# Kernel optimization log

Hardware: AMD Instinct MI355X
Metric: run time of the kernel (lower is better)

## Reference

```python
import jax, jax.numpy as jnp
import numpy as np
import math

B, S, D, H = 1, 2048, 4096, 32
HD = D // H
FF = 11008
EPS = 1e-5
THETA = 10000.0


def rms_norm(x, w, eps=EPS):
    # use_mean=False, elementwise_scale=True, high-precision pow -> RMSNorm in fp32
    xf = x.astype(jnp.float32)
    inv = jax.lax.rsqrt(jnp.mean(xf * xf, axis=-1, keepdims=True) + eps)
    return ((xf * inv).astype(x.dtype)) * w


def rope(x, theta=THETA):
    # x: [b, s, h, hd]; interleaved (adjacent-pair) rotary as in LLaMA/FMS
    s, hd = x.shape[1], x.shape[-1]
    inv_freq = 1.0 / (theta ** (jnp.arange(0, hd, 2, dtype=jnp.float32) / hd))
    ang = jnp.arange(s, dtype=jnp.float32)[:, None] * inv_freq[None, :]  # [s, hd/2]
    cos = jnp.cos(ang)[None, :, None, :].astype(x.dtype)
    sin = jnp.sin(ang)[None, :, None, :].astype(x.dtype)
    x1 = x[..., 0::2]
    x2 = x[..., 1::2]
    r1 = x1 * cos - x2 * sin
    r2 = x1 * sin + x2 * cos
    return jnp.stack([r1, r2], axis=-1).reshape(x.shape)


def block_forward(x, ln_w, ff_ln_w, wq, wk, wv, wo, wg, w1, w2):
    residual = x
    xn = rms_norm(x, ln_w)
    b, s, d = xn.shape
    q = rope((xn @ wq).reshape(b, s, H, HD))
    k = rope((xn @ wk).reshape(b, s, H, HD))
    v = (xn @ wv).reshape(b, s, H, HD)
    scores = jnp.einsum('bqhd,bkhd->bhqk', q, k) / math.sqrt(HD)
    causal = jnp.tril(jnp.ones((s, s), dtype=bool))
    scores = jnp.where(causal[None, None], scores, jnp.finfo(scores.dtype).min)
    probs = jax.nn.softmax(scores, axis=-1)
    attn = jnp.einsum('bhqk,bkhd->bqhd', probs, v).reshape(b, s, d)
    x = attn @ wo + residual

    residual = x
    xn = rms_norm(x, ff_ln_w)
    h = jax.nn.silu(xn @ wg) * (xn @ w1)  # swish-gated GLU
    x = h @ w2 + residual
    return x


def setup_inputs() -> dict:
    key = jax.random.key(0)
    ks = jax.random.split(key, 8)
    sc = lambda fan_in: 1.0 / math.sqrt(fan_in)
    return {
        'x': jax.random.normal(ks[0], (B, S, D), jnp.float32),
        'ln_w': jnp.ones((D,), jnp.float32),
        'ff_ln_w': jnp.ones((D,), jnp.float32),
        'wq': jax.random.normal(ks[1], (D, D), jnp.float32) * sc(D),
        'wk': jax.random.normal(ks[2], (D, D), jnp.float32) * sc(D),
        'wv': jax.random.normal(ks[3], (D, D), jnp.float32) * sc(D),
        'wo': jax.random.normal(ks[4], (D, D), jnp.float32) * sc(D),
        'wg': jax.random.normal(ks[5], (D, FF), jnp.float32) * sc(D),
        'w1': jax.random.normal(ks[6], (D, FF), jnp.float32) * sc(D),
        'w2': jax.random.normal(ks[7], (FF, D), jnp.float32) * sc(FF),
    }


def reference(x, ln_w, ff_ln_w, wq, wk, wv, wo, wg, w1, w2):
    return block_forward(x, ln_w, ff_ln_w, wq, wk, wv, wo, wg, w1, w2)
```

## Files before the change

kernel.cpp:

```cpp
#include <hip/hip_runtime.h>
#include <cstdint>
#include <cmath>


typedef unsigned short u16;
typedef unsigned int u32;
typedef __bf16 bf16x8 __attribute__((ext_vector_type(8)));
typedef float f32x4 __attribute__((ext_vector_type(4)));

__device__ __forceinline__ float bf2f(u16 u) {
    u32 x = ((u32)u) << 16; float f; __builtin_memcpy(&f, &x, 4); return f;
}
__device__ __forceinline__ u16 f2bf(float f) {
    u32 x; __builtin_memcpy(&x, &f, 4);
    u32 r = x + 0x7fff + ((x >> 16) & 1);
    return (u16)(r >> 16);
}

__device__ __forceinline__ void g2l16(const void* g, void* l) {
    auto* gp = reinterpret_cast<const u32*>(reinterpret_cast<uintptr_t>(g));
    auto* lp = reinterpret_cast<__attribute__((address_space(3))) u32*>(
        reinterpret_cast<uintptr_t>(l));
    __builtin_amdgcn_global_load_lds(gp, lp, 16, 0, 0);
}

__global__ __launch_bounds__(256) void transpose_f32_bf16(
    const float* __restrict__ in, u16* __restrict__ out, int K, int N) {
    __shared__ float tile[64][33];
    const int k0 = blockIdx.y * 64, n0 = blockIdx.x * 32;
    const int x = threadIdx.x, y = threadIdx.y;
#pragma unroll
    for (int i = 0; i < 8; i++) {
        int kr = y + i * 8;
        tile[kr][x] = in[(size_t)(k0 + kr) * N + n0 + x];
    }
    __syncthreads();
#pragma unroll
    for (int i = 0; i < 4; i++) {
        int nr = y + i * 8;
        u32 pk = (u32)f2bf(tile[2 * x][nr]) | ((u32)f2bf(tile[2 * x + 1][nr]) << 16);
        ((u32*)(out + (size_t)(n0 + nr) * K + k0))[x] = pk;
    }
}

__global__ __launch_bounds__(256) void rmsnorm_kernel(
    const float* __restrict__ x, const float* __restrict__ w, u16* __restrict__ o) {
    const int row = blockIdx.x;
    const float4* xr = (const float4*)(x + (size_t)row * 4096);
    float4 v[4];
    float ss = 0.f;
#pragma unroll
    for (int i = 0; i < 4; i++) {
        v[i] = xr[threadIdx.x + 256 * i];
        ss += v[i].x * v[i].x + v[i].y * v[i].y + v[i].z * v[i].z + v[i].w * v[i].w;
    }
#pragma unroll
    for (int off = 32; off > 0; off >>= 1) ss += __shfl_down(ss, off, 64);
    __shared__ float ws4[4];
    if ((threadIdx.x & 63) == 0) ws4[threadIdx.x >> 6] = ss;
    __syncthreads();
    float inv = rsqrtf((ws4[0] + ws4[1] + ws4[2] + ws4[3]) * (1.f / 4096.f) + 1e-5f);
    const float4* wr = (const float4*)w;
    u32* orow = (u32*)(o + (size_t)row * 4096);
#pragma unroll
    for (int i = 0; i < 4; i++) {
        float4 wv = wr[threadIdx.x + 256 * i];
        u32 lo = (u32)f2bf(v[i].x * inv * wv.x) | ((u32)f2bf(v[i].y * inv * wv.y) << 16);
        u32 hi = (u32)f2bf(v[i].z * inv * wv.z) | ((u32)f2bf(v[i].w * inv * wv.w) << 16);
        int idx = (threadIdx.x + 256 * i) * 2;
        orow[idx] = lo; orow[idx + 1] = hi;
    }
}

__global__ __launch_bounds__(256) void rope_kernel(u16* __restrict__ q, u16* __restrict__ k) {
    const int s = blockIdx.x;
    u32* pr = (u32*)((blockIdx.y ? k : q) + (size_t)s * 4096);
#pragma unroll
    for (int it = 0; it < 8; it++) {
        int pidx = threadIdx.x + it * 256;
        int i = pidx & 63;
        float ang = (float)s * expf(-(float)i * 0.14391156832817f);
        float sn, cs; sincosf(ang, &sn, &cs);
        u32 u = pr[pidx];
        float x1 = bf2f((u16)u), x2 = bf2f((u16)(u >> 16));
        pr[pidx] = (u32)f2bf(x1 * cs - x2 * sn) | ((u32)f2bf(x1 * sn + x2 * cs) << 16);
    }
}

__global__ __launch_bounds__(256) void silu_mul_kernel(
    const u16* __restrict__ g, const u16* __restrict__ u, u16* __restrict__ o) {
    size_t i = (size_t)blockIdx.x * 256 + threadIdx.x;
    uint4 gv = ((const uint4*)g)[i];
    uint4 uv = ((const uint4*)u)[i];
    const u32* gp = (const u32*)&gv;
    const u32* up = (const u32*)&uv;
    u32 rr[4];
#pragma unroll
    for (int j = 0; j < 4; j++) {
        float g0 = bf2f((u16)gp[j]), g1 = bf2f((u16)(gp[j] >> 16));
        float u0 = bf2f((u16)up[j]), u1 = bf2f((u16)(up[j] >> 16));
        float s0 = g0 / (1.f + __expf(-g0)) * u0;
        float s1 = g1 / (1.f + __expf(-g1)) * u1;
        rr[j] = (u32)f2bf(s0) | ((u32)f2bf(s1) << 16);
    }
    ((uint4*)o)[i] = *(const uint4*)rr;
}

template <int EPI>
__global__ __launch_bounds__(256) void gemm_bt(
    const u16* __restrict__ A, const u16* __restrict__ BT, void* __restrict__ Cout,
    const float* __restrict__ res, int M, int N, int K, int lda, int ldb, int ldc) {
    (void)M; (void)N;
    __shared__ u16 As[128 * 32];
    __shared__ u16 Bs[128 * 32];
    const int tid = threadIdx.x;
    const int lane = tid & 63, wave = tid >> 6;
    const int m0 = blockIdx.y * 128, n0 = blockIdx.x * 128;
    const int wm = (wave >> 1) * 64, wn = (wave & 1) * 64;
    const int gc = lane & 15, grp = lane >> 4;

    const u16* ga0 = A + (size_t)(m0 + (tid >> 2)) * lda + (tid & 3) * 8;
    const u16* ga1 = ga0 + (size_t)64 * lda;
    const u16* gb0 = BT + (size_t)(n0 + (tid >> 2)) * ldb + (tid & 3) * 8;
    const u16* gb1 = gb0 + (size_t)64 * ldb;
    u16* la0 = As + tid * 8;
    u16* la1 = As + tid * 8 + 2048;
    u16* lb0 = Bs + tid * 8;
    u16* lb1 = Bs + tid * 8 + 2048;

    f32x4 acc[4][4] = {};

    for (int k0 = 0; k0 < K; k0 += 32) {
        g2l16(ga0, la0); g2l16(ga1, la1);
        g2l16(gb0, lb0); g2l16(gb1, lb1);
        ga0 += 32; ga1 += 32; gb0 += 32; gb1 += 32;
        __syncthreads();
        bf16x8 af[4], bfr[4];
#pragma unroll
        for (int t = 0; t < 4; t++) {
            af[t]  = *(const bf16x8*)(As + (wm + t * 16 + gc) * 32 + grp * 8);
            bfr[t] = *(const bf16x8*)(Bs + (wn + t * 16 + gc) * 32 + grp * 8);
        }
#pragma unroll
        for (int mt = 0; mt < 4; mt++)
#pragma unroll
            for (int nt = 0; nt < 4; nt++)
                acc[mt][nt] = __builtin_amdgcn_mfma_f32_16x16x32_bf16(
                    af[mt], bfr[nt], acc[mt][nt], 0, 0, 0);
        __syncthreads();
    }

#pragma unroll
    for (int mt = 0; mt < 4; mt++) {
#pragma unroll
        for (int nt = 0; nt < 4; nt++) {
            int row0 = m0 + wm + mt * 16 + grp * 4;
            int col = n0 + wn + nt * 16 + gc;
            if (EPI == 0) {
                u16* C = (u16*)Cout;
#pragma unroll
                for (int r = 0; r < 4; r++)
                    C[(size_t)(row0 + r) * ldc + col] = f2bf(acc[mt][nt][r]);
            } else if (EPI == 1) {
                u16* C = (u16*)Cout;
                u32 p0 = (u32)f2bf(acc[mt][nt][0]) | ((u32)f2bf(acc[mt][nt][1]) << 16);
                u32 p1 = (u32)f2bf(acc[mt][nt][2]) | ((u32)f2bf(acc[mt][nt][3]) << 16);
                u32* dst = (u32*)(C + (size_t)col * ldc + row0);
                dst[0] = p0; dst[1] = p1;
            } else {
                float* C = (float*)Cout;
#pragma unroll
                for (int r = 0; r < 4; r++) {
                    size_t idx = (size_t)(row0 + r) * ldc + col;
                    C[idx] = acc[mt][nt][r] + res[idx];
                }
            }
        }
    }
}

__global__ __launch_bounds__(256) void attn_kernel(
    const u16* __restrict__ q, const u16* __restrict__ k,
    const u16* __restrict__ vt, u16* __restrict__ o) {
    __shared__ u16 Ks[64][136];
    __shared__ u16 Vs[128][72];
    __shared__ u16 Ps[128][72];
    const int h = blockIdx.y;
    const int m0 = blockIdx.x * 128;
    const int tid = threadIdx.x, lane = tid & 63, wave = tid >> 6;
    const int mw = m0 + wave * 32;
    const int gc = lane & 15, grp = lane >> 4;
    const float scale = 0.08838834764831843f;

    bf16x8 qf[2][4];
#pragma unroll
    for (int mt = 0; mt < 2; mt++)
#pragma unroll
        for (int ks = 0; ks < 4; ks++)
            qf[mt][ks] = *(const bf16x8*)(q + (size_t)(mw + mt * 16 + gc) * 4096 +
                                          h * 128 + ks * 32 + grp * 8);

    f32x4 oacc[2][8] = {};
    float mrun[2][4], lrun[2][4];
#pragma unroll
    for (int mt = 0; mt < 2; mt++)
#pragma unroll
        for (int r = 0; r < 4; r++) { mrun[mt][r] = -1e30f; lrun[mt][r] = 0.f; }

    const int jend = m0 + 128;
    for (int j0 = 0; j0 < jend; j0 += 64) {
#pragma unroll
        for (int i = 0; i < 4; i++) {
            int c = tid + i * 256;
            int kr = c >> 4, dc = (c & 15) * 8;
            *(uint4*)(&Ks[kr][dc]) =
                *(const uint4*)(k + (size_t)(j0 + kr) * 4096 + h * 128 + dc);
            int vr = c >> 3, vc = (c & 7) * 8;
            *(uint4*)(&Vs[vr][vc]) =
                *(const uint4*)(vt + (size_t)(h * 128 + vr) * 2048 + j0 + vc);
        }
        __syncthreads();

        f32x4 sfr[2][4] = {};
#pragma unroll
        for (int ks = 0; ks < 4; ks++) {
            bf16x8 kf[4];
#pragma unroll
            for (int nt = 0; nt < 4; nt++)
                kf[nt] = *(const bf16x8*)(&Ks[nt * 16 + gc][ks * 32 + grp * 8]);
#pragma unroll
            for (int mt = 0; mt < 2; mt++)
#pragma unroll
                for (int nt = 0; nt < 4; nt++)
                    sfr[mt][nt] = __builtin_amdgcn_mfma_f32_16x16x32_bf16(
                        qf[mt][ks], kf[nt], sfr[mt][nt], 0, 0, 0);
        }

        if (j0 + 63 > mw) {
#pragma unroll
            for (int mt = 0; mt < 2; mt++)
#pragma unroll
                for (int nt = 0; nt < 4; nt++)
#pragma unroll
                    for (int r = 0; r < 4; r++) {
                        int rowg = mw + mt * 16 + grp * 4 + r;
                        int colg = j0 + nt * 16 + gc;
                        if (colg > rowg) sfr[mt][nt][r] = -3.0e38f;
                    }
        }

#pragma unroll
        for (int mt = 0; mt < 2; mt++) {
#pragma unroll
            for (int r = 0; r < 4; r++) {
                float rm = fmaxf(fmaxf(sfr[mt][0][r], sfr[mt][1][r]),
                                 fmaxf(sfr[mt][2][r], sfr[mt][3][r])) * scale;
#pragma unroll
                for (int msk = 1; msk < 16; msk <<= 1)
                    rm = fmaxf(rm, __shfl_xor(rm, msk, 64));
                float mnew = fmaxf(mrun[mt][r], rm);
                float alpha = __expf(mrun[mt][r] - mnew);
                mrun[mt][r] = mnew;
                float rs = 0.f;
#pragma unroll
                for (int nt = 0; nt < 4; nt++) {
                    float pv = __expf(sfr[mt][nt][r] * scale - mnew);
                    sfr[mt][nt][r] = pv;
                    rs += pv;
                }
#pragma unroll
                for (int msk = 1; msk < 16; msk <<= 1) rs += __shfl_xor(rs, msk, 64);
                lrun[mt][r] = lrun[mt][r] * alpha + rs;
#pragma unroll
                for (int nd = 0; nd < 8; nd++) oacc[mt][nd][r] *= alpha;
            }
        }

#pragma unroll
        for (int mt = 0; mt < 2; mt++)
#pragma unroll
            for (int nt = 0; nt < 4; nt++)
#pragma unroll
                for (int r = 0; r < 4; r++)
                    Ps[wave * 32 + mt * 16 + grp * 4 + r][nt * 16 + gc] =
                        f2bf(sfr[mt][nt][r]);
        __syncthreads();

#pragma unroll
        for (int ks2 = 0; ks2 < 2; ks2++) {
            bf16x8 pf[2];
#pragma unroll
            for (int mt = 0; mt < 2; mt++)
                pf[mt] = *(const bf16x8*)(&Ps[wave * 32 + mt * 16 + gc][ks2 * 32 + grp * 8]);
#pragma unroll
            for (int nd = 0; nd < 8; nd++) {
                bf16x8 vf = *(const bf16x8*)(&Vs[nd * 16 + gc][ks2 * 32 + grp * 8]);
#pragma unroll
                for (int mt = 0; mt < 2; mt++)
                    oacc[mt][nd] = __builtin_amdgcn_mfma_f32_16x16x32_bf16(
                        pf[mt], vf, oacc[mt][nd], 0, 0, 0);
            }
        }
        __syncthreads();
    }

#pragma unroll
    for (int mt = 0; mt < 2; mt++)
#pragma unroll
        for (int r = 0; r < 4; r++) {
            float invl = 1.f / lrun[mt][r];
            int rowg = mw + mt * 16 + grp * 4 + r;
#pragma unroll
            for (int nd = 0; nd < 8; nd++)
                o[(size_t)rowg * 4096 + h * 128 + nd * 16 + gc] =
                    f2bf(oacc[mt][nd][r] * invl);
        }
}

extern "C" void kernel_launch(void* const* d_in, const int* in_sizes, int n_in,
                              void* d_out, int out_size, void* d_ws, size_t ws_size,
                              hipStream_t stream) {
    (void)in_sizes; (void)n_in; (void)out_size; (void)ws_size;
    const float* x    = (const float*)d_in[0];
    const float* ln_w = (const float*)d_in[1];
    const float* ffw  = (const float*)d_in[2];
    const float* wq   = (const float*)d_in[3];
    const float* wk   = (const float*)d_in[4];
    const float* wv   = (const float*)d_in[5];
    const float* wo   = (const float*)d_in[6];
    const float* wg   = (const float*)d_in[7];
    const float* w1   = (const float*)d_in[8];
    const float* w2   = (const float*)d_in[9];
    float* out = (float*)d_out;

    char* p = (char*)d_ws;
    auto alloc = [&](size_t n) { char* r = p; p += (n + 255) & ~(size_t)255; return r; };
    u16* wqT = (u16*)alloc((size_t)4096 * 4096 * 2);
    u16* wkT = (u16*)alloc((size_t)4096 * 4096 * 2);
    u16* wvT = (u16*)alloc((size_t)4096 * 4096 * 2);
    u16* woT = (u16*)alloc((size_t)4096 * 4096 * 2);
    u16* wgT = (u16*)alloc((size_t)11008 * 4096 * 2);
    u16* w1T = (u16*)alloc((size_t)11008 * 4096 * 2);
    u16* w2T = (u16*)alloc((size_t)4096 * 11008 * 2);
    u16* xn  = (u16*)alloc((size_t)2048 * 4096 * 2);
    u16* qb  = (u16*)alloc((size_t)2048 * 4096 * 2);
    u16* kb  = (u16*)alloc((size_t)2048 * 4096 * 2);
    u16* vtb = (u16*)alloc((size_t)4096 * 2048 * 2);
    u16* ab  = (u16*)alloc((size_t)2048 * 4096 * 2);
    float* x2 = (float*)alloc((size_t)2048 * 4096 * 4);
    u16* xn2 = (u16*)alloc((size_t)2048 * 4096 * 2);
    u16* gb  = (u16*)alloc((size_t)2048 * 11008 * 2);
    u16* ub  = (u16*)alloc((size_t)2048 * 11008 * 2);

    dim3 tb(32, 8);
    transpose_f32_bf16<<<dim3(128, 64), tb, 0, stream>>>(wq, wqT, 4096, 4096);
    transpose_f32_bf16<<<dim3(128, 64), tb, 0, stream>>>(wk, wkT, 4096, 4096);
    transpose_f32_bf16<<<dim3(128, 64), tb, 0, stream>>>(wv, wvT, 4096, 4096);
    transpose_f32_bf16<<<dim3(128, 64), tb, 0, stream>>>(wo, woT, 4096, 4096);
    transpose_f32_bf16<<<dim3(344, 64), tb, 0, stream>>>(wg, wgT, 4096, 11008);
    transpose_f32_bf16<<<dim3(344, 64), tb, 0, stream>>>(w1, w1T, 4096, 11008);
    transpose_f32_bf16<<<dim3(128, 172), tb, 0, stream>>>(w2, w2T, 11008, 4096);

    rmsnorm_kernel<<<2048, 256, 0, stream>>>(x, ln_w, xn);

    gemm_bt<0><<<dim3(32, 16), 256, 0, stream>>>(xn, wqT, qb, nullptr,
                                                 2048, 4096, 4096, 4096, 4096, 4096);
    gemm_bt<0><<<dim3(32, 16), 256, 0, stream>>>(xn, wkT, kb, nullptr,
                                                 2048, 4096, 4096, 4096, 4096, 4096);
    gemm_bt<1><<<dim3(32, 16), 256, 0, stream>>>(xn, wvT, vtb, nullptr,
                                                 2048, 4096, 4096, 4096, 4096, 2048);

    rope_kernel<<<dim3(2048, 2), 256, 0, stream>>>(qb, kb);

    attn_kernel<<<dim3(16, 32), 256, 0, stream>>>(qb, kb, vtb, ab);

    gemm_bt<2><<<dim3(32, 16), 256, 0, stream>>>(ab, woT, x2, x,
                                                 2048, 4096, 4096, 4096, 4096, 4096);

    rmsnorm_kernel<<<2048, 256, 0, stream>>>(x2, ffw, xn2);

    gemm_bt<0><<<dim3(86, 16), 256, 0, stream>>>(xn2, wgT, gb, nullptr,
                                                 2048, 11008, 4096, 4096, 4096, 11008);
    gemm_bt<0><<<dim3(86, 16), 256, 0, stream>>>(xn2, w1T, ub, nullptr,
                                                 2048, 11008, 4096, 4096, 4096, 11008);

    silu_mul_kernel<<<11008, 256, 0, stream>>>(gb, ub, gb);

    gemm_bt<2><<<dim3(32, 16), 256, 0, stream>>>(gb, w2T, out, x2,
                                                 2048, 4096, 11008, 11008, 11008, 4096);
}
```

Before: 2.421 ms.

## Pair causal attention tiles per block with double-buffered K/V and 8 waves

The attention kernel now gives each block two query tiles (ti and 15-ti), so every block does a roughly equal amount of causal work. It uses 512 threads with 16 rows per wave and double-buffers K/V in shared memory, loading the next tile into registers while the current one is computed. This also drops one barrier per iteration. The aim is to remove load imbalance from the causal mask and hide global load latency, at the cost of more shared memory and half as many blocks (256) on the device.

```diff
diff --git a/kernel.cpp b/kernel.cpp
--- a/kernel.cpp
+++ b/kernel.cpp
@@ -179,142 +179,166 @@
     }
 }
 
-__global__ __launch_bounds__(256) void attn_kernel(
+__global__ __launch_bounds__(512) void attn_kernel(
     const u16* __restrict__ q, const u16* __restrict__ k,
     const u16* __restrict__ vt, u16* __restrict__ o) {
-    __shared__ u16 Ks[64][136];
-    __shared__ u16 Vs[128][72];
+    __shared__ u16 Ks[2][64][136];
+    __shared__ u16 Vs[2][128][72];
     __shared__ u16 Ps[128][72];
     const int h = blockIdx.y;
-    const int m0 = blockIdx.x * 128;
     const int tid = threadIdx.x, lane = tid & 63, wave = tid >> 6;
-    const int mw = m0 + wave * 32;
     const int gc = lane & 15, grp = lane >> 4;
     const float scale = 0.08838834764831843f;
 
-    bf16x8 qf[2][4];
-#pragma unroll
-    for (int mt = 0; mt < 2; mt++)
-#pragma unroll
-        for (int ks = 0; ks < 4; ks++)
-            qf[mt][ks] = *(const bf16x8*)(q + (size_t)(mw + mt * 16 + gc) * 4096 +
-                                          h * 128 + ks * 32 + grp * 8);
-
-    f32x4 oacc[2][8] = {};
-    float mrun[2][4], lrun[2][4];
-#pragma unroll
-    for (int mt = 0; mt < 2; mt++)
-#pragma unroll
-        for (int r = 0; r < 4; r++) { mrun[mt][r] = -1e30f; lrun[mt][r] = 0.f; }
-
-    const int jend = m0 + 128;
-    for (int j0 = 0; j0 < jend; j0 += 64) {
-#pragma unroll
-        for (int i = 0; i < 4; i++) {
-            int c = tid + i * 256;
-            int kr = c >> 4, dc = (c & 15) * 8;
-            *(uint4*)(&Ks[kr][dc]) =
-                *(const uint4*)(k + (size_t)(j0 + kr) * 4096 + h * 128 + dc);
-            int vr = c >> 3, vc = (c & 7) * 8;
-            *(uint4*)(&Vs[vr][vc]) =
-                *(const uint4*)(vt + (size_t)(h * 128 + vr) * 2048 + j0 + vc);
-        }
-        __syncthreads();
-
-        f32x4 sfr[2][4] = {};
+    const int ti0 = blockIdx.x;
+    const int ti1 = 15 - (int)blockIdx.x;
+    const int n0 = 2 * ti0 + 2;
+    const int total = n0 + 2 * ti1 + 2;
+
+    {
+        uint4 kr0[2], vr0[2];
+#pragma unroll
+        for (int i = 0; i < 2; i++) {
+            int c = tid + i * 512;
+            kr0[i] = *(const uint4*)(k + (size_t)(c >> 4) * 4096 + h * 128 + (c & 15) * 8);
+            vr0[i] = *(const uint4*)(vt + (size_t)(h * 128 + (c >> 3)) * 2048 + (c & 7) * 8);
+        }
+#pragma unroll
+        for (int i = 0; i < 2; i++) {
+            int c = tid + i * 512;
+            *(uint4*)(&Ks[0][c >> 4][(c & 15) * 8]) = kr0[i];
+            *(uint4*)(&Vs[0][c >> 3][(c & 7) * 8]) = vr0[i];
+        }
+    }
+    __syncthreads();
+
+    bf16x8 qf[4];
+    f32x4 oacc[8];
+    float mrun[4], lrun[4];
+    const f32x4 fzero = {};
+    int cur = 0;
+
+    for (int it = 0; it < total; ++it) {
+        const int t = (it >= n0) ? 1 : 0;
+        const int local = t ? it - n0 : it;
+        const int ti = t ? ti1 : ti0;
+        const int j0 = local * 64;
+        const int mw = ti * 128 + wave * 16;
+
+        if (local == 0) {
+#pragma unroll
+            for (int ks = 0; ks < 4; ks++)
+                qf[ks] = *(const bf16x8*)(q + (size_t)(mw + gc) * 4096 + h * 128 +
+                                          ks * 32 + grp * 8);
+#pragma unroll
+            for (int nd = 0; nd < 8; nd++) oacc[nd] = fzero;
+#pragma unroll
+            for (int r = 0; r < 4; r++) { mrun[r] = -1e30f; lrun[r] = 0.f; }
+        }
+
+        const int itn = it + 1;
+        const bool havenext = itn < total;
+        const int jn = (itn >= n0 ? itn - n0 : itn) * 64;
+        uint4 kreg[2], vreg[2];
+        if (havenext) {
+#pragma unroll
+            for (int i = 0; i < 2; i++) {
+                int c = tid + i * 512;
+                kreg[i] = *(const uint4*)(k + (size_t)(jn + (c >> 4)) * 4096 +
+                                          h * 128 + (c & 15) * 8);
+                vreg[i] = *(const uint4*)(vt + (size_t)(h * 128 + (c >> 3)) * 2048 +
+                                          jn + (c & 7) * 8);
+            }
+        }
+
+        f32x4 sfr[4] = {};
 #pragma unroll
         for (int ks = 0; ks < 4; ks++) {
             bf16x8 kf[4];
 #pragma unroll
             for (int nt = 0; nt < 4; nt++)
-                kf[nt] = *(const bf16x8*)(&Ks[nt * 16 + gc][ks * 32 + grp * 8]);
-#pragma unroll
-            for (int mt = 0; mt < 2; mt++)
-#pragma unroll
-                for (int nt = 0; nt < 4; nt++)
-                    sfr[mt][nt] = __builtin_amdgcn_mfma_f32_16x16x32_bf16(
-                        qf[mt][ks], kf[nt], sfr[mt][nt], 0, 0, 0);
+                kf[nt] = *(const bf16x8*)(&Ks[cur][nt * 16 + gc][ks * 32 + grp * 8]);
+#pragma unroll
+            for (int nt = 0; nt < 4; nt++)
+                sfr[nt] = __builtin_amdgcn_mfma_f32_16x16x32_bf16(
+                    qf[ks], kf[nt], sfr[nt], 0, 0, 0);
         }
 
         if (j0 + 63 > mw) {
 #pragma unroll
-            for (int mt = 0; mt < 2; mt++)
-#pragma unroll
-                for (int nt = 0; nt < 4; nt++)
-#pragma unroll
-                    for (int r = 0; r < 4; r++) {
-                        int rowg = mw + mt * 16 + grp * 4 + r;
-                        int colg = j0 + nt * 16 + gc;
-                        if (colg > rowg) sfr[mt][nt][r] = -3.0e38f;
-                    }
-        }
-
-#pragma unroll
-        for (int mt = 0; mt < 2; mt++) {
+            for (int nt = 0; nt < 4; nt++)
+#pragma unroll
+                for (int r = 0; r < 4; r++) {
+                    int rowg = mw + grp * 4 + r;
+                    int colg = j0 + nt * 16 + gc;
+                    if (colg > rowg) sfr[nt][r] = -3.0e38f;
+                }
+        }
+
+#pragma unroll
+        for (int r = 0; r < 4; r++) {
+            float rm = fmaxf(fmaxf(sfr[0][r], sfr[1][r]),
+                             fmaxf(sfr[2][r], sfr[3][r])) * scale;
+#pragma unroll
+            for (int msk = 1; msk < 16; msk <<= 1)
+                rm = fmaxf(rm, __shfl_xor(rm, msk, 64));
+            float mnew = fmaxf(mrun[r], rm);
+            float alpha = __expf(mrun[r] - mnew);
+            mrun[r] = mnew;
+            float rs = 0.f;
+#pragma unroll
+            for (int nt = 0; nt < 4; nt++) {
+                float pv = __expf(sfr[nt][r] * scale - mnew);
+                sfr[nt][r] = pv;
+                rs += pv;
+            }
+#pragma unroll
+            for (int msk = 1; msk < 16; msk <<= 1) rs += __shfl_xor(rs, msk, 64);
+            lrun[r] = lrun[r] * alpha + rs;
+#pragma unroll
+            for (int nd = 0; nd < 8; nd++) oacc[nd][r] *= alpha;
+        }
+
+#pragma unroll
+        for (int nt = 0; nt < 4; nt++)
+#pragma unroll
+            for (int r = 0; r < 4; r++)
+                Ps[wave * 16 + grp * 4 + r][nt * 16 + gc] = f2bf(sfr[nt][r]);
+
+#pragma unroll
+        for (int ks2 = 0; ks2 < 2; ks2++) {
+            bf16x8 pf = *(const bf16x8*)(&Ps[wave * 16 + gc][ks2 * 32 + grp * 8]);
+#pragma unroll
+            for (int nd = 0; nd < 8; nd++) {
+                bf16x8 vf = *(const bf16x8*)(&Vs[cur][nd * 16 + gc][ks2 * 32 + grp * 8]);
+                oacc[nd] = __builtin_amdgcn_mfma_f32_16x16x32_bf16(
+                    pf, vf, oacc[nd], 0, 0, 0);
+            }
+        }
+
+        if (havenext) {
+#pragma unroll
+            for (int i = 0; i < 2; i++) {
+                int c = tid + i * 512;
+                *(uint4*)(&Ks[cur ^ 1][c >> 4][(c & 15) * 8]) = kreg[i];
+                *(uint4*)(&Vs[cur ^ 1][c >> 3][(c & 7) * 8]) = vreg[i];
+            }
+        }
+        __syncthreads();
+        cur ^= 1;
+
+        if (local == 2 * ti + 1) {
 #pragma unroll
             for (int r = 0; r < 4; r++) {
-                float rm = fmaxf(fmaxf(sfr[mt][0][r], sfr[mt][1][r]),
-                                 fmaxf(sfr[mt][2][r], sfr[mt][3][r])) * scale;
-#pragma unroll
-                for (int msk = 1; msk < 16; msk <<= 1)
-                    rm = fmaxf(rm, __shfl_xor(rm, msk, 64));
-                float mnew = fmaxf(mrun[mt][r], rm);
-                float alpha = __expf(mrun[mt][r] - mnew);
-                mrun[mt][r] = mnew;
-                float rs = 0.f;
-#pragma unroll
-                for (int nt = 0; nt < 4; nt++) {
-                    float pv = __expf(sfr[mt][nt][r] * scale - mnew);
-                    sfr[mt][nt][r] = pv;
-                    rs += pv;
-                }
-#pragma unroll
-                for (int msk = 1; msk < 16; msk <<= 1) rs += __shfl_xor(rs, msk, 64);
-                lrun[mt][r] = lrun[mt][r] * alpha + rs;
-#pragma unroll
-                for (int nd = 0; nd < 8; nd++) oacc[mt][nd][r] *= alpha;
-            }
-        }
-
-#pragma unroll
-        for (int mt = 0; mt < 2; mt++)
-#pragma unroll
-            for (int nt = 0; nt < 4; nt++)
-#pragma unroll
-                for (int r = 0; r < 4; r++)
-                    Ps[wave * 32 + mt * 16 + grp * 4 + r][nt * 16 + gc] =
-                        f2bf(sfr[mt][nt][r]);
-        __syncthreads();
-
-#pragma unroll
-        for (int ks2 = 0; ks2 < 2; ks2++) {
-            bf16x8 pf[2];
-#pragma unroll
-            for (int mt = 0; mt < 2; mt++)
-                pf[mt] = *(const bf16x8*)(&Ps[wave * 32 + mt * 16 + gc][ks2 * 32 + grp * 8]);
-#pragma unroll
-            for (int nd = 0; nd < 8; nd++) {
-                bf16x8 vf = *(const bf16x8*)(&Vs[nd * 16 + gc][ks2 * 32 + grp * 8]);
-#pragma unroll
-                for (int mt = 0; mt < 2; mt++)
-                    oacc[mt][nd] = __builtin_amdgcn_mfma_f32_16x16x32_bf16(
-                        pf[mt], vf, oacc[mt][nd], 0, 0, 0);
-            }
-        }
-        __syncthreads();
-    }
-
-#pragma unroll
-    for (int mt = 0; mt < 2; mt++)
-#pragma unroll
-        for (int r = 0; r < 4; r++) {
-            float invl = 1.f / lrun[mt][r];
-            int rowg = mw + mt * 16 + grp * 4 + r;
-#pragma unroll
-            for (int nd = 0; nd < 8; nd++)
-                o[(size_t)rowg * 4096 + h * 128 + nd * 16 + gc] =
-                    f2bf(oacc[mt][nd][r] * invl);
-        }
+                float invl = 1.f / lrun[r];
+                int rowg = mw + grp * 4 + r;
+#pragma unroll
+                for (int nd = 0; nd < 8; nd++)
+                    o[(size_t)rowg * 4096 + h * 128 + nd * 16 + gc] =
+                        f2bf(oacc[nd][r] * invl);
+            }
+        }
+    }
 }
 
 extern "C" void kernel_launch(void* const* d_in, const int* in_sizes, int n_in,
@@ -372,7 +396,7 @@
 
     rope_kernel<<<dim3(2048, 2), 256, 0, stream>>>(qb, kb);
 
-    attn_kernel<<<dim3(16, 32), 256, 0, stream>>>(qb, kb, vtb, ab);
+    attn_kernel<<<dim3(8, 32), 512, 0, stream>>>(qb, kb, vtb, ab);
 
     gemm_bt<2><<<dim3(32, 16), 256, 0, stream>>>(ab, woT, x2, x,
                                                  2048, 4096, 4096, 4096, 4096, 4096);
```

After: 2.231 ms. 1.08x faster.
